# Kernel optimization log

Measured on AMD Instinct MI355X. Metric: run time of the kernel, lower is better.

The kernel has to match this reference:

```python
import jax, jax.numpy as jnp
import numpy as np

N = 131072
H = 768

def setup_inputs() -> dict:
    key = jax.random.key(0)
    k1, k2, k3, k4 = jax.random.split(key, 4)
    h_i = jax.random.normal(k1, (N, H), dtype=jnp.float32)
    W_weight = jax.random.normal(k2, (H, H), dtype=jnp.float32) * 0.02
    W_bias = jax.random.normal(k3, (H,), dtype=jnp.float32) * 0.02
    v = jax.random.normal(k4, (1, H), dtype=jnp.float32) * 0.1
    return {"h_i": h_i, "W_weight": W_weight, "W_bias": W_bias, "v": v}

def reference(h_i, W_weight, W_bias, v):
    # u_i = tanh(Linear(h_i)) : [N, H]
    u_i = jnp.tanh(h_i @ W_weight.T + W_bias)
    # scores = v @ u_i.T : [1, N]
    scores = v @ u_i.T
    alpha = jax.nn.softmax(scores, axis=1)  # [1, N]
    # weighted sum over N -> [1, H]
    return alpha @ h_i
```

## Files before the change

kernel.cpp:

```cpp
#include <hip/hip_runtime.h>

#define HDIM 768
#define BM 64
#define NCHUNK 24
#define CHUNK_BYTES 49152
#define A_STRIDE 1552

typedef _Float16 f16x8 __attribute__((ext_vector_type(8)));
typedef _Float16 f16x4 __attribute__((ext_vector_type(4)));
typedef float f32x4 __attribute__((ext_vector_type(4)));

#define LDS_B     99328
#define LDS_BIAS  (LDS_B + CHUNK_BYTES)
#define LDS_V     (LDS_BIAS + 3072)
#define LDS_TOTAL (LDS_V + 3072)

#define WS_WT    0
#define WS_Z     1179648
#define WS_PART  1179712
#define WS_PART2 7471168
#define WS_NEED  (WS_PART2 + 49152)

__device__ __forceinline__ float tanh_fast(float z) {
    float e2 = __expf(2.0f * z);
    return 1.0f - 2.0f / (e2 + 1.0f);
}

__device__ __forceinline__ void stage16(const void* g, void* l) {
    __builtin_amdgcn_global_load_lds(
        (const __attribute__((address_space(1))) void*)g,
        (__attribute__((address_space(3))) void*)l, 16, 0, 0);
}

__global__ __launch_bounds__(1024) void prep_kernel(
    const float* __restrict__ W, _Float16* __restrict__ Wt,
    float* __restrict__ Z, float* __restrict__ accbuf) {
    int idx = blockIdx.x * 1024 + threadIdx.x;
    if (idx < HDIM * HDIM / 4) {
        int j  = idx / 192;
        int r  = idx - j * 192;
        int kc = r >> 3;
        int k4 = r & 7;
        f32x4 x = *(const f32x4*)(W + j * HDIM + kc * 32 + k4 * 4);
        f16x4 v;
        v[0] = (_Float16)x[0]; v[1] = (_Float16)x[1];
        v[2] = (_Float16)x[2]; v[3] = (_Float16)x[3];
        *(f16x4*)(Wt + kc * 24576 + j * 32 + k4 * 4) = v;
    }
    if (idx < HDIM) accbuf[idx] = 0.0f;
    if (idx == 0) *Z = 0.0f;
}

__global__ __launch_bounds__(1024, 2) void score_fused_kernel(
    const float* __restrict__ h, const _Float16* __restrict__ Wt,
    const float* __restrict__ bias, const float* __restrict__ vvec,
    float* __restrict__ part, float* __restrict__ accbuf,
    float* __restrict__ Z, int use_part) {

    extern __shared__ char smem[];
    float* bias_s = (float*)(smem + LDS_BIAS);
    float* v_s    = (float*)(smem + LDS_V);
    float* s_red  = (float*)(smem + LDS_B);
    float* e_lds  = (float*)(smem + LDS_B + 4096);

    const int tid  = threadIdx.x;
    const int wave = tid >> 6;
    const int lane = tid & 63;
    const int l15  = lane & 15;
    const int lhi  = lane >> 4;
    const int row0 = blockIdx.x * BM;

    if (tid < HDIM) { bias_s[tid] = bias[tid]; v_s[tid] = vvec[tid]; }

    {
        const char* g = (const char*)Wt;
        #pragma unroll
        for (int s = 0; s < 3; ++s) {
            int idx = wave * 3 + s;
            stage16(g + idx * 1024 + lane * 16, smem + LDS_B + idx * 1024);
        }
    }
    if (tid < 512) {
        int r = tid >> 3, k4 = tid & 7;
        f32x4 x = *(const f32x4*)(h + (size_t)(row0 + r) * HDIM + k4 * 4);
        f16x4 v;
        v[0] = (_Float16)x[0]; v[1] = (_Float16)x[1];
        v[2] = (_Float16)x[2]; v[3] = (_Float16)x[3];
        *(f16x4*)(smem + r * A_STRIDE + k4 * 8) = v;
    }
    __syncthreads();

    f32x4 acc[4][3];
    #pragma unroll
    for (int rt = 0; rt < 4; ++rt)
        #pragma unroll
        for (int ct = 0; ct < 3; ++ct)
            acc[rt][ct] = (f32x4){0.f, 0.f, 0.f, 0.f};

    const char* bbase0 = smem + LDS_B + (wave * 48 + l15) * 64 + lhi * 16;
    const char* abase0 = smem + l15 * A_STRIDE + lhi * 16;

    for (int kc = 0; kc < NCHUNK; ++kc) {
        f32x4 pb0, pb1, pb2, pa;
        const bool has = (kc + 1 < NCHUNK);
        if (has) {
            const char* src = (const char*)Wt + (size_t)(kc + 1) * CHUNK_BYTES;
            pb0 = *(const f32x4*)(src + 0 * 16384 + tid * 16);
            pb1 = *(const f32x4*)(src + 1 * 16384 + tid * 16);
            pb2 = *(const f32x4*)(src + 2 * 16384 + tid * 16);
            if (tid < 512)
                pa = *(const f32x4*)(h + (size_t)(row0 + (tid >> 3)) * HDIM
                                       + (kc + 1) * 32 + (tid & 7) * 4);
        }
        const char* bb = bbase0;
        f16x8 b0 = *(const f16x8*)(bb);
        f16x8 b1 = *(const f16x8*)(bb + 1024);
        f16x8 b2 = *(const f16x8*)(bb + 2048);
        const char* ab = abase0 + kc * 64;
        #pragma unroll
        for (int rt = 0; rt < 4; ++rt) {
            f16x8 av = *(const f16x8*)(ab + rt * (16 * A_STRIDE));
            acc[rt][0] = __builtin_amdgcn_mfma_f32_16x16x32_f16(av, b0, acc[rt][0], 0, 0, 0);
            acc[rt][1] = __builtin_amdgcn_mfma_f32_16x16x32_f16(av, b1, acc[rt][1], 0, 0, 0);
            acc[rt][2] = __builtin_amdgcn_mfma_f32_16x16x32_f16(av, b2, acc[rt][2], 0, 0, 0);
        }
        __syncthreads();
        if (has) {
            *(f32x4*)(smem + LDS_B + 0 * 16384 + tid * 16) = pb0;
            *(f32x4*)(smem + LDS_B + 1 * 16384 + tid * 16) = pb1;
            *(f32x4*)(smem + LDS_B + 2 * 16384 + tid * 16) = pb2;
            if (tid < 512) {
                f16x4 v;
                v[0] = (_Float16)pa[0]; v[1] = (_Float16)pa[1];
                v[2] = (_Float16)pa[2]; v[3] = (_Float16)pa[3];
                *(f16x4*)(smem + (tid >> 3) * A_STRIDE + (kc + 1) * 64 + (tid & 7) * 8) = v;
            }
            __syncthreads();
        }
    }

    float pr[4][4];
    #pragma unroll
    for (int rt = 0; rt < 4; ++rt)
        #pragma unroll
        for (int r = 0; r < 4; ++r) pr[rt][r] = 0.f;

    #pragma unroll
    for (int ct = 0; ct < 3; ++ct) {
        int col = wave * 48 + ct * 16 + l15;
        float bj = bias_s[col];
        float vj = v_s[col];
        #pragma unroll
        for (int rt = 0; rt < 4; ++rt)
            #pragma unroll
            for (int r = 0; r < 4; ++r)
                pr[rt][r] = fmaf(vj, tanh_fast(acc[rt][ct][r] + bj), pr[rt][r]);
    }
    #pragma unroll
    for (int rt = 0; rt < 4; ++rt)
        #pragma unroll
        for (int r = 0; r < 4; ++r) {
            float x = pr[rt][r];
            x += __shfl_xor(x, 1);
            x += __shfl_xor(x, 2);
            x += __shfl_xor(x, 4);
            x += __shfl_xor(x, 8);
            if (l15 == 0) s_red[wave * 64 + rt * 16 + lhi * 4 + r] = x;
        }
    __syncthreads();

    if (tid < 64) {
        float s = 0.f;
        #pragma unroll
        for (int w = 0; w < 16; ++w) s += s_red[w * 64 + tid];
        float e = __expf(s);
        e_lds[tid] = e;
        float tot = e;
        tot += __shfl_xor(tot, 1);
        tot += __shfl_xor(tot, 2);
        tot += __shfl_xor(tot, 4);
        tot += __shfl_xor(tot, 8);
        tot += __shfl_xor(tot, 16);
        tot += __shfl_xor(tot, 32);
        if (tid == 0) atomicAdd(Z, tot);
    }
    __syncthreads();

    if (tid < HDIM) {
        const _Float16* A = (const _Float16*)smem;
        float s = 0.f;
        #pragma unroll 8
        for (int i = 0; i < BM; ++i)
            s += e_lds[i] * (float)A[i * 776 + tid];
        if (use_part) part[(size_t)blockIdx.x * HDIM + tid] = s;
        else          atomicAdd(accbuf + tid, s);
    }
}

__global__ __launch_bounds__(128) void fin1_kernel(
    const float* __restrict__ part, float* __restrict__ part2) {
    const int g  = blockIdx.x / 6;
    const int cb = blockIdx.x % 6;
    const int col = cb * 128 + threadIdx.x;
    float s = 0.f;
    #pragma unroll 8
    for (int p = g * 128; p < (g + 1) * 128; ++p) s += part[(size_t)p * HDIM + col];
    part2[g * HDIM + col] = s;
}

__global__ __launch_bounds__(128) void fin2_kernel(
    const float* __restrict__ src, const float* __restrict__ Z,
    float* __restrict__ out, int ngroups) {
    const int col = blockIdx.x * 128 + threadIdx.x;
    float s = 0.f;
    for (int g = 0; g < ngroups; ++g) s += src[g * HDIM + col];
    out[col] = s / (*Z);
}

extern "C" void kernel_launch(void* const* d_in, const int* in_sizes, int n_in,
                              void* d_out, int out_size, void* d_ws, size_t ws_size,
                              hipStream_t stream) {
    const float* h    = (const float*)d_in[0];
    const float* W    = (const float*)d_in[1];
    const float* bias = (const float*)d_in[2];
    const float* vv   = (const float*)d_in[3];
    float* out = (float*)d_out;

    const int n = in_sizes[0] / HDIM;

    char* ws = (char*)d_ws;
    _Float16* Wt  = (_Float16*)(ws + WS_WT);
    float* Z      = (float*)(ws + WS_Z);
    float* part   = (float*)(ws + WS_PART);
    float* part2  = (float*)(ws + WS_PART2);
    float* accbuf = (float*)(ws + WS_PART);

    const int use_part = (ws_size >= (size_t)WS_NEED) ? 1 : 0;

    hipFuncSetAttribute((const void*)score_fused_kernel,
                        hipFuncAttributeMaxDynamicSharedMemorySize, LDS_TOTAL);

    prep_kernel<<<144, 1024, 0, stream>>>(W, Wt, Z, accbuf);

    score_fused_kernel<<<n / BM, 1024, LDS_TOTAL, stream>>>(
        h, Wt, bias, vv, part, accbuf, Z, use_part);

    if (use_part) {
        fin1_kernel<<<96, 128, 0, stream>>>(part, part2);
        fin2_kernel<<<HDIM / 128, 128, 0, stream>>>(part2, Z, out, 16);
    } else {
        fin2_kernel<<<HDIM / 128, 128, 0, stream>>>(accbuf, Z, out, 1);
    }
}
```

Baseline: 345.7 us.

## Double-buffer W chunks via direct-to-LDS loads and stream h rows through registers

The W^T chunks are now double-buffered in LDS with async global_load_lds, so the per-chunk register round-trip and the second barrier go away. The h tiles are loaded straight into registers, one chunk ahead, and converted to fp16 for the MFMA operands instead of being staged in LDS. The B layout gets an XOR swizzle to cut LDS bank conflicts, and the launch bound moves to 4 blocks. The final weighted sum now re-reads h in fp32 from global memory, which adds traffic that L2 may or may not absorb. The tighter launch bound also risks register pressure or spills.

Result: slower. 959.2 us (+177.5%).

```diff
diff --git a/kernel.cpp b/kernel.cpp
--- a/kernel.cpp
+++ b/kernel.cpp
@@ -3,17 +3,18 @@
 #define HDIM 768
 #define BM 64
 #define NCHUNK 24
-#define CHUNK_BYTES 49152
-#define A_STRIDE 1552
+#define CHUNK_B 49152
 
 typedef _Float16 f16x8 __attribute__((ext_vector_type(8)));
-typedef _Float16 f16x4 __attribute__((ext_vector_type(4)));
 typedef float f32x4 __attribute__((ext_vector_type(4)));
 
-#define LDS_B     99328
-#define LDS_BIAS  (LDS_B + CHUNK_BYTES)
-#define LDS_V     (LDS_BIAS + 3072)
-#define LDS_TOTAL (LDS_V + 3072)
+#define LDS_BUF0 0
+#define LDS_BUF1 49152
+#define LDS_BIAS 98304
+#define LDS_V    101376
+#define LDS_SRED 104448
+#define LDS_E    108544
+#define LDS_TOTAL 108864
 
 #define WS_WT    0
 #define WS_Z     1179648
@@ -32,26 +33,36 @@
         (__attribute__((address_space(3))) void*)l, 16, 0, 0);
 }
 
+__device__ __forceinline__ f16x8 cvt8(f32x4 x0, f32x4 x1) {
+    f16x8 f;
+    f[0] = (_Float16)x0[0]; f[1] = (_Float16)x0[1];
+    f[2] = (_Float16)x0[2]; f[3] = (_Float16)x0[3];
+    f[4] = (_Float16)x1[0]; f[5] = (_Float16)x1[1];
+    f[6] = (_Float16)x1[2]; f[7] = (_Float16)x1[3];
+    return f;
+}
+
 __global__ __launch_bounds__(1024) void prep_kernel(
     const float* __restrict__ W, _Float16* __restrict__ Wt,
     float* __restrict__ Z, float* __restrict__ accbuf) {
     int idx = blockIdx.x * 1024 + threadIdx.x;
-    if (idx < HDIM * HDIM / 4) {
-        int j  = idx / 192;
-        int r  = idx - j * 192;
-        int kc = r >> 3;
-        int k4 = r & 7;
-        f32x4 x = *(const f32x4*)(W + j * HDIM + kc * 32 + k4 * 4);
-        f16x4 v;
-        v[0] = (_Float16)x[0]; v[1] = (_Float16)x[1];
-        v[2] = (_Float16)x[2]; v[3] = (_Float16)x[3];
-        *(f16x4*)(Wt + kc * 24576 + j * 32 + k4 * 4) = v;
+    if (idx < 73728) {
+        int c  = idx / 96;
+        int r  = idx - c * 96;
+        int kc = r >> 2;
+        int q  = r & 3;
+        const float* src = W + c * HDIM + kc * 32 + q * 8;
+        f32x4 x0 = *(const f32x4*)src;
+        f32x4 x1 = *(const f32x4*)(src + 4);
+        f16x8 v = cvt8(x0, x1);
+        int qs = q ^ ((c >> 1) & 3);
+        *(f16x8*)((char*)Wt + (size_t)kc * CHUNK_B + c * 64 + qs * 16) = v;
     }
     if (idx < HDIM) accbuf[idx] = 0.0f;
     if (idx == 0) *Z = 0.0f;
 }
 
-__global__ __launch_bounds__(1024, 2) void score_fused_kernel(
+__global__ __launch_bounds__(1024, 4) void score_fused_kernel(
     const float* __restrict__ h, const _Float16* __restrict__ Wt,
     const float* __restrict__ bias, const float* __restrict__ vvec,
     float* __restrict__ part, float* __restrict__ accbuf,
@@ -60,8 +71,8 @@
     extern __shared__ char smem[];
     float* bias_s = (float*)(smem + LDS_BIAS);
     float* v_s    = (float*)(smem + LDS_V);
-    float* s_red  = (float*)(smem + LDS_B);
-    float* e_lds  = (float*)(smem + LDS_B + 4096);
+    float* s_red  = (float*)(smem + LDS_SRED);
+    float* e_lds  = (float*)(smem + LDS_E);
 
     const int tid  = threadIdx.x;
     const int wave = tid >> 6;
@@ -72,22 +83,23 @@
 
     if (tid < HDIM) { bias_s[tid] = bias[tid]; v_s[tid] = vvec[tid]; }
 
-    {
-        const char* g = (const char*)Wt;
-        #pragma unroll
-        for (int s = 0; s < 3; ++s) {
-            int idx = wave * 3 + s;
-            stage16(g + idx * 1024 + lane * 16, smem + LDS_B + idx * 1024);
-        }
-    }
-    if (tid < 512) {
-        int r = tid >> 3, k4 = tid & 7;
-        f32x4 x = *(const f32x4*)(h + (size_t)(row0 + r) * HDIM + k4 * 4);
-        f16x4 v;
-        v[0] = (_Float16)x[0]; v[1] = (_Float16)x[1];
-        v[2] = (_Float16)x[2]; v[3] = (_Float16)x[3];
-        *(f16x4*)(smem + r * A_STRIDE + k4 * 8) = v;
-    }
+    const int quad = lhi ^ ((l15 >> 1) & 3);
+    const int boff = (wave * 48 + l15) * 64 + quad * 16;
+
+    #pragma unroll
+    for (int s = 0; s < 3; ++s) {
+        int idx = wave * 3 + s;
+        stage16((const char*)Wt + idx * 1024 + lane * 16, smem + LDS_BUF0 + idx * 1024);
+    }
+
+    const size_t abase = (size_t)(row0 + l15) * HDIM + lhi * 8;
+    f32x4 aP[8];
+    #pragma unroll
+    for (int rt = 0; rt < 4; ++rt) {
+        aP[2 * rt]     = *(const f32x4*)(h + abase + (size_t)rt * 16 * HDIM);
+        aP[2 * rt + 1] = *(const f32x4*)(h + abase + (size_t)rt * 16 * HDIM + 4);
+    }
+
     __syncthreads();
 
     f32x4 acc[4][3];
@@ -97,46 +109,46 @@
         for (int ct = 0; ct < 3; ++ct)
             acc[rt][ct] = (f32x4){0.f, 0.f, 0.f, 0.f};
 
-    const char* bbase0 = smem + LDS_B + (wave * 48 + l15) * 64 + lhi * 16;
-    const char* abase0 = smem + l15 * A_STRIDE + lhi * 16;
-
     for (int kc = 0; kc < NCHUNK; ++kc) {
-        f32x4 pb0, pb1, pb2, pa;
-        const bool has = (kc + 1 < NCHUNK);
-        if (has) {
-            const char* src = (const char*)Wt + (size_t)(kc + 1) * CHUNK_BYTES;
-            pb0 = *(const f32x4*)(src + 0 * 16384 + tid * 16);
-            pb1 = *(const f32x4*)(src + 1 * 16384 + tid * 16);
-            pb2 = *(const f32x4*)(src + 2 * 16384 + tid * 16);
-            if (tid < 512)
-                pa = *(const f32x4*)(h + (size_t)(row0 + (tid >> 3)) * HDIM
-                                       + (kc + 1) * 32 + (tid & 7) * 4);
+        const int cb = (kc & 1) ? LDS_BUF1 : LDS_BUF0;
+        if (kc + 1 < NCHUNK) {
+            const char* g = (const char*)Wt + (size_t)(kc + 1) * CHUNK_B;
+            char* d = smem + ((kc & 1) ? LDS_BUF0 : LDS_BUF1);
+            #pragma unroll
+            for (int s = 0; s < 3; ++s) {
+                int idx = wave * 3 + s;
+                stage16(g + idx * 1024 + lane * 16, d + idx * 1024);
+            }
         }
-        const char* bb = bbase0;
+        f16x8 af0 = cvt8(aP[0], aP[1]);
+        f16x8 af1 = cvt8(aP[2], aP[3]);
+        f16x8 af2 = cvt8(aP[4], aP[5]);
+        f16x8 af3 = cvt8(aP[6], aP[7]);
+        if (kc + 1 < NCHUNK) {
+            const float* hp = h + abase + (size_t)(kc + 1) * 32;
+            #pragma unroll
+            for (int rt = 0; rt < 4; ++rt) {
+                aP[2 * rt]     = *(const f32x4*)(hp + (size_t)rt * 16 * HDIM);
+                aP[2 * rt + 1] = *(const f32x4*)(hp + (size_t)rt * 16 * HDIM + 4);
+            }
+        }
+        const char* bb = smem + cb + boff;
         f16x8 b0 = *(const f16x8*)(bb);
         f16x8 b1 = *(const f16x8*)(bb + 1024);
         f16x8 b2 = *(const f16x8*)(bb + 2048);
-        const char* ab = abase0 + kc * 64;
-        #pragma unroll
-        for (int rt = 0; rt < 4; ++rt) {
-            f16x8 av = *(const f16x8*)(ab + rt * (16 * A_STRIDE));
-            acc[rt][0] = __builtin_amdgcn_mfma_f32_16x16x32_f16(av, b0, acc[rt][0], 0, 0, 0);
-            acc[rt][1] = __builtin_amdgcn_mfma_f32_16x16x32_f16(av, b1, acc[rt][1], 0, 0, 0);
-            acc[rt][2] = __builtin_amdgcn_mfma_f32_16x16x32_f16(av, b2, acc[rt][2], 0, 0, 0);
-        }
+        acc[0][0] = __builtin_amdgcn_mfma_f32_16x16x32_f16(af0, b0, acc[0][0], 0, 0, 0);
+        acc[0][1] = __builtin_amdgcn_mfma_f32_16x16x32_f16(af0, b1, acc[0][1], 0, 0, 0);
+        acc[0][2] = __builtin_amdgcn_mfma_f32_16x16x32_f16(af0, b2, acc[0][2], 0, 0, 0);
+        acc[1][0] = __builtin_amdgcn_mfma_f32_16x16x32_f16(af1, b0, acc[1][0], 0, 0, 0);
+        acc[1][1] = __builtin_amdgcn_mfma_f32_16x16x32_f16(af1, b1, acc[1][1], 0, 0, 0);
+        acc[1][2] = __builtin_amdgcn_mfma_f32_16x16x32_f16(af1, b2, acc[1][2], 0, 0, 0);
+        acc[2][0] = __builtin_amdgcn_mfma_f32_16x16x32_f16(af2, b0, acc[2][0], 0, 0, 0);
+        acc[2][1] = __builtin_amdgcn_mfma_f32_16x16x32_f16(af2, b1, acc[2][1], 0, 0, 0);
+        acc[2][2] = __builtin_amdgcn_mfma_f32_16x16x32_f16(af2, b2, acc[2][2], 0, 0, 0);
+        acc[3][0] = __builtin_amdgcn_mfma_f32_16x16x32_f16(af3, b0, acc[3][0], 0, 0, 0);
+        acc[3][1] = __builtin_amdgcn_mfma_f32_16x16x32_f16(af3, b1, acc[3][1], 0, 0, 0);
+        acc[3][2] = __builtin_amdgcn_mfma_f32_16x16x32_f16(af3, b2, acc[3][2], 0, 0, 0);
         __syncthreads();
-        if (has) {
-            *(f32x4*)(smem + LDS_B + 0 * 16384 + tid * 16) = pb0;
-            *(f32x4*)(smem + LDS_B + 1 * 16384 + tid * 16) = pb1;
-            *(f32x4*)(smem + LDS_B + 2 * 16384 + tid * 16) = pb2;
-            if (tid < 512) {
-                f16x4 v;
-                v[0] = (_Float16)pa[0]; v[1] = (_Float16)pa[1];
-                v[2] = (_Float16)pa[2]; v[3] = (_Float16)pa[3];
-                *(f16x4*)(smem + (tid >> 3) * A_STRIDE + (kc + 1) * 64 + (tid & 7) * 8) = v;
-            }
-            __syncthreads();
-        }
     }
 
     float pr[4][4];
@@ -187,11 +199,10 @@
     __syncthreads();
 
     if (tid < HDIM) {
-        const _Float16* A = (const _Float16*)smem;
         float s = 0.f;
         #pragma unroll 8
         for (int i = 0; i < BM; ++i)
-            s += e_lds[i] * (float)A[i * 776 + tid];
+            s += e_lds[i] * h[(size_t)(row0 + i) * HDIM + tid];
         if (use_part) part[(size_t)blockIdx.x * HDIM + tid] = s;
         else          atomicAdd(accbuf + tid, s);
     }
@@ -240,7 +251,7 @@
     hipFuncSetAttribute((const void*)score_fused_kernel,
                         hipFuncAttributeMaxDynamicSharedMemorySize, LDS_TOTAL);
 
-    prep_kernel<<<144, 1024, 0, stream>>>(W, Wt, Z, accbuf);
+    prep_kernel<<<72, 1024, 0, stream>>>(W, Wt, Z, accbuf);
 
     score_fused_kernel<<<n / BM, 1024, LDS_TOTAL, stream>>>(
         h, Wt, bias, vv, part, accbuf, Z, use_part);
```
